# Performance work log

Measured on AMD Instinct MI355X. Metric: run time of the kernel, lower is better.

Reference implementation:

```python
import jax, jax.numpy as jnp
import numpy as np

IS_DECODER = True
NEG = -100000.0


def setup_inputs() -> dict:
    key = jax.random.key(0)
    ks = jax.random.split(key, 8)
    B, S, E, H = 8, 2048, 1024, 64
    return {
        "hidden_state": jax.random.normal(ks[0], (B, S, E), dtype=jnp.float32),
        "attention_masks": jax.random.randint(ks[1], (B, S), 0, 2, dtype=jnp.int32),
        "Wq": jax.random.normal(ks[2], (E, H), dtype=jnp.float32) / np.sqrt(E),
        "bq": jax.random.normal(ks[3], (H,), dtype=jnp.float32) * 0.02,
        "Wk": jax.random.normal(ks[4], (E, H), dtype=jnp.float32) / np.sqrt(E),
        "bk": jax.random.normal(ks[5], (H,), dtype=jnp.float32) * 0.02,
        "Wv": jax.random.normal(ks[6], (E, H), dtype=jnp.float32) / np.sqrt(E),
        "bv": jax.random.normal(ks[7], (H,), dtype=jnp.float32) * 0.02,
    }


def reference(hidden_state, attention_masks, Wq, bq, Wk, bk, Wv, bv):
    # projections: q,k,v [B,S,H]
    q = hidden_state @ Wq + bq
    k = hidden_state @ Wk + bk
    v = hidden_state @ Wv + bv
    dim = q.shape[-1]
    # scores [B,S,S]
    score = jnp.einsum("bqh,bkh->bqk", q, k) / jnp.sqrt(jnp.float32(dim))
    m = attention_masks.astype(score.dtype)  # [B,S]
    pad = 1.0 - m
    amm = m[:, :, None] * m[:, None, :]      # [B,S,S]
    pmm = pad[:, :, None] * pad[:, None, :]
    if IS_DECODER:
        S = m.shape[-1]
        amm = amm * jnp.tril(jnp.ones((S, S), dtype=score.dtype))
    coupling = 1.0 - amm - pmm
    score = score + coupling * NEG
    weights = jax.nn.softmax(score, axis=-1)
    return jnp.einsum("bqk,bkh->bqh", weights, v)
```

## Files before the change

### kernel.cpp

```cpp
#include <hip/hip_runtime.h>

typedef float f32x4 __attribute__((ext_vector_type(4)));
typedef float f32x16 __attribute__((ext_vector_type(16)));
typedef unsigned int u32x4 __attribute__((ext_vector_type(4)));
typedef __bf16 bf16x8 __attribute__((ext_vector_type(8)));
typedef unsigned short ushort_t;

#define NEG2 (-144269.5f)
#define SCLQ (0.18033688f)

constexpr int Ss = 2048, Ee = 1024, Hh = 64;

static __device__ __forceinline__ ushort_t f2bfu(float f) {
  return __builtin_bit_cast(ushort_t, (__bf16)f);
}
static __device__ __forceinline__ f32x4 mfma16(bf16x8 a, bf16x8 b, f32x4 c) {
  return __builtin_amdgcn_mfma_f32_16x16x32_bf16(a, b, c, 0, 0, 0);
}
static __device__ __forceinline__ f32x16 mfma32(bf16x8 a, bf16x8 b, f32x16 c) {
  return __builtin_amdgcn_mfma_f32_32x32x16_bf16(a, b, c, 0, 0, 0);
}
static __device__ __forceinline__ unsigned cvtpk(float a, float b) {
  unsigned r;
  asm("v_cvt_pk_bf16_f32 %0, %1, %2" : "=v"(r) : "v"(a), "v"(b));
  return r;
}
static __device__ __forceinline__ void swap32(unsigned& a, unsigned& b) {
  asm("v_permlane32_swap_b32 %0, %1" : "+v"(a), "+v"(b));
}
static __device__ __forceinline__ void gload_lds16(const void* g, void* l) {
  __builtin_amdgcn_global_load_lds(
      (const __attribute__((address_space(1))) unsigned int*)g,
      (__attribute__((address_space(3))) unsigned int*)l, 16, 0, 0);
}


__global__ __launch_bounds__(256) void k_wtrans(const float* __restrict__ Wq,
                                                const float* __restrict__ Wk,
                                                const float* __restrict__ Wv,
                                                ushort_t* __restrict__ Wsw) {
  __shared__ float tile[64][65];
  const float* W = (blockIdx.y == 0) ? Wq : (blockIdx.y == 1 ? Wk : Wv);
  int kt = blockIdx.x, t = threadIdx.x;
  int r = t >> 2, cq = t & 3;
  const float* src = W + (kt * 64 + r) * Hh + cq * 16;
#pragma unroll
  for (int j = 0; j < 16; j += 4) {
    float4 v = *reinterpret_cast<const float4*>(src + j);
    tile[r][cq * 16 + j + 0] = v.x;
    tile[r][cq * 16 + j + 1] = v.y;
    tile[r][cq * 16 + j + 2] = v.z;
    tile[r][cq * 16 + j + 3] = v.w;
  }
  __syncthreads();
  int n = t >> 2, kq = t & 3;
  int rr = blockIdx.y * 64 + n;
  ushort_t ob[16];
#pragma unroll
  for (int j = 0; j < 16; ++j) ob[j] = f2bfu(tile[kq * 16 + j][n]);
#pragma unroll
  for (int j = 0; j < 2; ++j) {
    int c16 = 2 * kq + j;
    size_t off = ((size_t)(kt * 192 + rr)) * 64 + (size_t)(((c16 ^ (rr & 7))) * 8);
    *reinterpret_cast<uint4*>(Wsw + off) = reinterpret_cast<uint4*>(ob)[j];
  }
}

__global__ __launch_bounds__(256, 2) void k_proj(const float* __restrict__ hs,
                                                 const float* __restrict__ bq,
                                                 const float* __restrict__ bk,
                                                 const float* __restrict__ bv,
                                                 const ushort_t* __restrict__ Wsw,
                                                 const int* __restrict__ am,
                                                 ushort_t* __restrict__ qf_,
                                                 ushort_t* __restrict__ kf_,
                                                 ushort_t* __restrict__ vf_,
                                                 float* __restrict__ pen) {
  __shared__ __align__(16) ushort_t bufA[2][32][72];
  __shared__ __align__(16) ushort_t bufW[2][192 * 64];

  int t = threadIdx.x, w = t >> 6, l = t & 63, g = l >> 4, c = l & 15;
  int wm = w >> 1, wn = w & 1;
  int row0 = blockIdx.x * 32;

  int ar = t >> 3, ach = t & 7;
  const float* agp = hs + (size_t)(row0 + ar) * Ee + ach * 8;

  f32x4 acc[6];
#pragma unroll
  for (int nt = 0; nt < 6; ++nt) acc[nt] = f32x4{0.f, 0.f, 0.f, 0.f};
  float4 aR0, aR1;

  auto LOADA = [&](int kk) {
    aR0 = *reinterpret_cast<const float4*>(agp + kk);
    aR1 = *reinterpret_cast<const float4*>(agp + kk + 4);
  };
  auto WRITEA = [&](int buf) {
    bf16x8 av;
    av[0] = (__bf16)aR0.x; av[1] = (__bf16)aR0.y; av[2] = (__bf16)aR0.z; av[3] = (__bf16)aR0.w;
    av[4] = (__bf16)aR1.x; av[5] = (__bf16)aR1.y; av[6] = (__bf16)aR1.z; av[7] = (__bf16)aR1.w;
    *reinterpret_cast<bf16x8*>(&bufA[buf][ar][ach * 8]) = av;
  };
  auto GLW = [&](int buf, int s) {
    const ushort_t* base = Wsw + (size_t)s * 12288;
#pragma unroll
    for (int j = 0; j < 6; ++j) {
      int seg = j * 4 + w;
      const ushort_t* gp = base + seg * 512 + l * 8;
      gload_lds16(gp, &bufW[buf][seg * 512]);
    }
  };
  auto COMPUTE = [&](int buf) {
    const ushort_t* Ab = &bufA[buf][wm * 16 + c][0];
    bf16x8 af0 = *reinterpret_cast<const bf16x8*>(Ab + g * 8);
    bf16x8 af1 = *reinterpret_cast<const bf16x8*>(Ab + 32 + g * 8);
#pragma unroll
    for (int nt = 0; nt < 6; ++nt) {
      int r = wn * 96 + nt * 16 + c;
      int slot = g ^ (r & 7);
      const ushort_t* Wb = &bufW[buf][r * 64];
      bf16x8 b0 = *reinterpret_cast<const bf16x8*>(Wb + slot * 8);
      bf16x8 b1 = *reinterpret_cast<const bf16x8*>(Wb + (slot ^ 4) * 8);
      acc[nt] = mfma16(af0, b0, acc[nt]);
      acc[nt] = mfma16(af1, b1, acc[nt]);
    }
  };

  LOADA(0);
  WRITEA(0);
  GLW(0, 0);
  LOADA(64);
  __builtin_amdgcn_sched_barrier(0);

  int cur = 0;
  for (int s = 0; s < 16; ++s) {
    __syncthreads();
    if (s < 15) {
      WRITEA(cur ^ 1);
      GLW(cur ^ 1, s + 1);
    }
    if (s < 14) {
      LOADA((s + 2) * 64);
      __builtin_amdgcn_sched_barrier(0);
    }
    COMPUTE(cur);
    cur ^= 1;
  }

#pragma unroll
  for (int nt = 0; nt < 6; ++nt) {
    int T = wn * 6 + nt;
    int m = T >> 2;
    int h = (T & 3) * 16 + c;
    const float* bias = (m == 0) ? bq : ((m == 1) ? bk : bv);
    float bb = bias[h];
    int cc = h >> 4, hh = (h >> 3) & 1, jj = h & 7;
    int dt = h >> 5, dl = h & 31;
#pragma unroll
    for (int i = 0; i < 4; ++i) {
      int row = row0 + wm * 16 + g * 4 + i;
      float val = acc[nt][i] + bb;
      int bi = row >> 11, rl = row & 2047;
      if (m == 0) {
        size_t a = ((((size_t)(bi * 64 + (rl >> 5)) * 4 + cc) * 2 + hh) * 32 + (rl & 31)) * 8 + jj;
        qf_[a] = f2bfu(val * SCLQ);
      } else if (m == 1) {
        size_t a = ((((size_t)(bi * 64 + (rl >> 5)) * 4 + cc) * 2 + hh) * 32 + (rl & 31)) * 8 + jj;
        kf_[a] = f2bfu(val);
      } else {
        int s16 = rl >> 4, vh = (rl >> 3) & 1, vj = rl & 7;
        size_t a = ((((size_t)(bi * 128 + s16) * 2 + dt) * 2 + vh) * 32 + dl) * 8 + vj;
        vf_[a] = f2bfu(val);
      }
    }
  }

  if (t < 32) {
    int grow = row0 + t;
    int bi = grow >> 11, s2 = grow & 2047;
    int mv = am[grow];
    pen[((size_t)bi * 2 + 0) * Ss + s2] = mv ? 0.f : NEG2;
    pen[((size_t)bi * 2 + 1) * Ss + s2] = mv ? NEG2 : 0.f;
  }
}

__global__ __launch_bounds__(256, 2) void k_attn(const ushort_t* __restrict__ qs,
                                                 const ushort_t* __restrict__ km,
                                                 const ushort_t* __restrict__ vm,
                                                 const int* __restrict__ am,
                                                 const float* __restrict__ pen,
                                                 float* __restrict__ opart,
                                                 float* __restrict__ lpart) {
  __shared__ float obuf[4][64][68];
  __shared__ float lls[4][64];

  int t = threadIdx.x, w = t >> 6, l = t & 63, lo = l & 31, hi = l >> 5;
  int bid = blockIdx.x;
  int b = bid & 7, qt2 = (bid >> 3) & 31, kh = bid >> 8;
  int q0A = qt2 * 64, q0B = q0A + 32;

  const size_t laneoff = (size_t)hi * 256 + lo * 8;

  const ushort_t* qbaseA = qs + (size_t)(b * 64 + qt2 * 2) * 2048 + laneoff;
  const ushort_t* qbaseB = qbaseA + 2048;
  bf16x8 qfA[4], qfB[4];
#pragma unroll
  for (int c = 0; c < 4; ++c) {
    qfA[c] = *reinterpret_cast<const bf16x8*>(qbaseA + (size_t)c * 512);
    qfB[c] = *reinterpret_cast<const bf16x8*>(qbaseB + (size_t)c * 512);
  }

  int mqA = am[b * Ss + q0A + lo], mqB = am[b * Ss + q0B + lo];
  float negqA = mqA ? NEG2 : 0.f, negqB = mqB ? NEG2 : 0.f;
  const float* pselA = pen + ((size_t)b * 2 + (mqA ? 0 : 1)) * Ss;
  const float* pselB = pen + ((size_t)b * 2 + (mqB ? 0 : 1)) * Ss;

  float llA = 0.f, llB = 0.f;
  f32x16 o0A = {0.f, 0.f, 0.f, 0.f, 0.f, 0.f, 0.f, 0.f, 0.f, 0.f, 0.f, 0.f, 0.f, 0.f, 0.f, 0.f};
  f32x16 o1A = o0A, o0B = o0A, o1B = o0A;
  const f32x16 z16 = o0A;

  const int kvbeg = kh * 1024 + w * 256;
  const ushort_t* kb = km + (size_t)b * 131072 + laneoff;
  const ushort_t* vb = vm + (size_t)b * 131072 + laneoff;

  for (int it = 0; it < 8; ++it) {
    const int kv0 = kvbeg + it * 32;
    const int kt32 = kv0 >> 5, s16 = kv0 >> 4;

    const ushort_t* kfp = kb + (size_t)kt32 * 2048;
    bf16x8 kf0 = *reinterpret_cast<const bf16x8*>(kfp);
    bf16x8 kf1 = *reinterpret_cast<const bf16x8*>(kfp + 512);
    bf16x8 kf2 = *reinterpret_cast<const bf16x8*>(kfp + 1024);
    bf16x8 kf3 = *reinterpret_cast<const bf16x8*>(kfp + 1536);
    const ushort_t* vfp = vb + (size_t)s16 * 1024;
    bf16x8 vf00 = *reinterpret_cast<const bf16x8*>(vfp);
    bf16x8 vf01 = *reinterpret_cast<const bf16x8*>(vfp + 512);
    bf16x8 vf10 = *reinterpret_cast<const bf16x8*>(vfp + 1024);
    bf16x8 vf11 = *reinterpret_cast<const bf16x8*>(vfp + 1536);

    f32x4 pvA[4];
#pragma unroll
    for (int j = 0; j < 4; ++j)
      pvA[j] = *reinterpret_cast<const f32x4*>(pselA + kv0 + j * 8 + hi * 4);

    f32x16 scA = mfma32(kf0, qfA[0], z16);
    scA = mfma32(kf1, qfA[1], scA);
    scA = mfma32(kf2, qfA[2], scA);
    scA = mfma32(kf3, qfA[3], scA);
    f32x16 scB = mfma32(kf0, qfB[0], z16);
    scB = mfma32(kf1, qfB[1], scB);
    scB = mfma32(kf2, qfB[2], scB);
    scB = mfma32(kf3, qfB[3], scB);

    if (kv0 == q0A) {
#pragma unroll
      for (int r = 0; r < 16; ++r) {
        int kr = (r & 3) + 8 * (r >> 2) + 4 * hi;
        scA[r] += pvA[r >> 2][r & 3] + ((kr > lo) ? negqA : 0.f);
      }
    } else {
      float addt = (kv0 > q0A) ? negqA : 0.f;
#pragma unroll
      for (int r = 0; r < 16; ++r) scA[r] += pvA[r >> 2][r & 3] + addt;
    }
    float pA[16], tsA = 0.f;
#pragma unroll
    for (int r = 0; r < 16; ++r) {
      pA[r] = __builtin_amdgcn_exp2f(scA[r]);
      tsA += pA[r];
    }
    llA += tsA;
    unsigned xa0 = cvtpk(pA[0], pA[1]), ya0 = cvtpk(pA[2], pA[3]);
    unsigned za0 = cvtpk(pA[4], pA[5]), wa0 = cvtpk(pA[6], pA[7]);
    swap32(xa0, za0);
    swap32(ya0, wa0);
    unsigned xa1 = cvtpk(pA[8], pA[9]), ya1 = cvtpk(pA[10], pA[11]);
    unsigned za1 = cvtpk(pA[12], pA[13]), wa1 = cvtpk(pA[14], pA[15]);
    swap32(xa1, za1);
    swap32(ya1, wa1);
    bf16x8 paA0 = __builtin_bit_cast(bf16x8, u32x4{xa0, ya0, za0, wa0});
    bf16x8 paA1 = __builtin_bit_cast(bf16x8, u32x4{xa1, ya1, za1, wa1});
    o0A = mfma32(paA0, vf00, o0A);
    o0A = mfma32(paA1, vf10, o0A);
    o1A = mfma32(paA0, vf01, o1A);
    o1A = mfma32(paA1, vf11, o1A);

    f32x4 pvB[4];
#pragma unroll
    for (int j = 0; j < 4; ++j)
      pvB[j] = *reinterpret_cast<const f32x4*>(pselB + kv0 + j * 8 + hi * 4);

    if (kv0 == q0B) {
#pragma unroll
      for (int r = 0; r < 16; ++r) {
        int kr = (r & 3) + 8 * (r >> 2) + 4 * hi;
        scB[r] += pvB[r >> 2][r & 3] + ((kr > lo) ? negqB : 0.f);
      }
    } else {
      float addt = (kv0 > q0B) ? negqB : 0.f;
#pragma unroll
      for (int r = 0; r < 16; ++r) scB[r] += pvB[r >> 2][r & 3] + addt;
    }
    float pB[16], tsB = 0.f;
#pragma unroll
    for (int r = 0; r < 16; ++r) {
      pB[r] = __builtin_amdgcn_exp2f(scB[r]);
      tsB += pB[r];
    }
    llB += tsB;
    unsigned xb0 = cvtpk(pB[0], pB[1]), yb0 = cvtpk(pB[2], pB[3]);
    unsigned zb0 = cvtpk(pB[4], pB[5]), wb0 = cvtpk(pB[6], pB[7]);
    swap32(xb0, zb0);
    swap32(yb0, wb0);
    unsigned xb1 = cvtpk(pB[8], pB[9]), yb1 = cvtpk(pB[10], pB[11]);
    unsigned zb1 = cvtpk(pB[12], pB[13]), wb1 = cvtpk(pB[14], pB[15]);
    swap32(xb1, zb1);
    swap32(yb1, wb1);
    bf16x8 paB0 = __builtin_bit_cast(bf16x8, u32x4{xb0, yb0, zb0, wb0});
    bf16x8 paB1 = __builtin_bit_cast(bf16x8, u32x4{xb1, yb1, zb1, wb1});
    o0B = mfma32(paB0, vf00, o0B);
    o0B = mfma32(paB1, vf10, o0B);
    o1B = mfma32(paB0, vf01, o1B);
    o1B = mfma32(paB1, vf11, o1B);
  }

  llA += __shfl_xor(llA, 32);
  llB += __shfl_xor(llB, 32);

#pragma unroll
  for (int r = 0; r < 16; ++r) {
    int qrow = (r & 3) + 8 * (r >> 2) + 4 * hi;
    obuf[w][qrow][lo] = o0A[r];
    obuf[w][qrow][32 + lo] = o1A[r];
    obuf[w][32 + qrow][lo] = o0B[r];
    obuf[w][32 + qrow][32 + lo] = o1B[r];
  }
  if (hi == 0) {
    lls[w][lo] = llA;
    lls[w][32 + lo] = llB;
  }
  __syncthreads();

  int qr = t >> 3, dg = t & 7;
#pragma unroll
  for (int pass = 0; pass < 2; ++pass) {
    int row = pass * 32 + qr;
    float lg = lls[0][row] + lls[1][row] + lls[2][row] + lls[3][row];
    float a8[8] = {0.f, 0.f, 0.f, 0.f, 0.f, 0.f, 0.f, 0.f};
#pragma unroll
    for (int ww = 0; ww < 4; ++ww) {
      float4 c0 = *reinterpret_cast<const float4*>(&obuf[ww][row][dg * 8]);
      float4 c1 = *reinterpret_cast<const float4*>(&obuf[ww][row][dg * 8 + 4]);
      a8[0] += c0.x; a8[1] += c0.y; a8[2] += c0.z; a8[3] += c0.w;
      a8[4] += c1.x; a8[5] += c1.y; a8[6] += c1.z; a8[7] += c1.w;
    }
    float* op = opart + (((size_t)kh * 8 + b) * Ss + q0A + row) * 64 + dg * 8;
    float4 r0v = {a8[0], a8[1], a8[2], a8[3]};
    float4 r1v = {a8[4], a8[5], a8[6], a8[7]};
    *reinterpret_cast<float4*>(op) = r0v;
    *reinterpret_cast<float4*>(op + 4) = r1v;
    if (dg == 0) lpart[((size_t)kh * 8 + b) * Ss + q0A + row] = lg;
  }
}

__global__ __launch_bounds__(256) void k_fin(const float* __restrict__ op,
                                             const float* __restrict__ lp,
                                             float* __restrict__ out) {
  int gi = blockIdx.x * 256 + threadIdx.x;
  int row = gi >> 4;
  float lsum = lp[row] + lp[row + 16384];
  f32x4 a = reinterpret_cast<const f32x4*>(op)[gi];
  f32x4 b = reinterpret_cast<const f32x4*>(op)[gi + 262144];
  float inv = 1.f / lsum;
  f32x4 r = (a + b) * inv;
  reinterpret_cast<f32x4*>(out)[gi] = r;
}

extern "C" void kernel_launch(void* const* d_in, const int* in_sizes, int n_in,
                              void* d_out, int out_size, void* d_ws, size_t ws_size,
                              hipStream_t stream) {
  const float* hs = (const float*)d_in[0];
  const int* am = (const int*)d_in[1];
  const float* Wq = (const float*)d_in[2];
  const float* bq = (const float*)d_in[3];
  const float* Wk = (const float*)d_in[4];
  const float* bk = (const float*)d_in[5];
  const float* Wv = (const float*)d_in[6];
  const float* bv = (const float*)d_in[7];
  float* out = (float*)d_out;

  char* ws = (char*)d_ws;
  ushort_t* qsp = (ushort_t*)(ws + 0);
  ushort_t* kp = (ushort_t*)(ws + (2u << 20));
  ushort_t* vtp = (ushort_t*)(ws + (4u << 20));
  ushort_t* wtp = (ushort_t*)(ws + (6u << 20));
  float* penp = (float*)(ws + (6u << 20) + (512u << 10));
  float* opart = (float*)(ws + (8u << 20));
  float* lpart = (float*)(ws + (16u << 20));

  k_wtrans<<<dim3(16, 3), 256, 0, stream>>>(Wq, Wk, Wv, wtp);
  k_proj<<<dim3(512), 256, 0, stream>>>(hs, bq, bk, bv, wtp, am, qsp, kp, vtp, penp);
  k_attn<<<dim3(512), 256, 0, stream>>>(qsp, kp, vtp, am, penp, opart, lpart);
  k_fin<<<dim3(1024), 256, 0, stream>>>(opart, lpart, out);
}
```

Before: 47.36 us.

## Fuse split-KV finalize into attention kernel using 8-wave blocks

Instead of splitting the KV range across two blocks and combining the partial outputs in a separate finalize kernel, each block now runs 8 waves covering the full 2048-long KV range. The partial outputs are reduced in shared memory in two stages, and the normalized result is written directly to the output. This removes one kernel launch and the global round-trip of the partial output and row-sum buffers. In exchange the grid is halved to 256 blocks of 512 threads, which may lower occupancy and adds an extra barrier plus a shared-memory accumulate step.

Measured after the change: 44.70 us (median of 2 runs). 5.6% less time.

```diff
diff --git a/kernel.cpp b/kernel.cpp
--- a/kernel.cpp
+++ b/kernel.cpp
@@ -184,19 +184,18 @@
   }
 }
 
-__global__ __launch_bounds__(256, 2) void k_attn(const ushort_t* __restrict__ qs,
+__global__ __launch_bounds__(512, 2) void k_attn(const ushort_t* __restrict__ qs,
                                                  const ushort_t* __restrict__ km,
                                                  const ushort_t* __restrict__ vm,
                                                  const int* __restrict__ am,
                                                  const float* __restrict__ pen,
-                                                 float* __restrict__ opart,
-                                                 float* __restrict__ lpart) {
+                                                 float* __restrict__ out) {
   __shared__ float obuf[4][64][68];
-  __shared__ float lls[4][64];
+  __shared__ float lls[8][64];
 
   int t = threadIdx.x, w = t >> 6, l = t & 63, lo = l & 31, hi = l >> 5;
   int bid = blockIdx.x;
-  int b = bid & 7, qt2 = (bid >> 3) & 31, kh = bid >> 8;
+  int b = bid & 7, qt2 = bid >> 3;
   int q0A = qt2 * 64, q0B = q0A + 32;
 
   const size_t laneoff = (size_t)hi * 256 + lo * 8;
@@ -220,7 +219,7 @@
   f32x16 o1A = o0A, o0B = o0A, o1B = o0A;
   const f32x16 z16 = o0A;
 
-  const int kvbeg = kh * 1024 + w * 256;
+  const int kvbeg = w * 256;
   const ushort_t* kb = km + (size_t)b * 131072 + laneoff;
   const ushort_t* vb = vm + (size_t)b * 131072 + laneoff;
 
@@ -327,54 +326,52 @@
 
   llA += __shfl_xor(llA, 32);
   llB += __shfl_xor(llB, 32);
-
-#pragma unroll
-  for (int r = 0; r < 16; ++r) {
-    int qrow = (r & 3) + 8 * (r >> 2) + 4 * hi;
-    obuf[w][qrow][lo] = o0A[r];
-    obuf[w][qrow][32 + lo] = o1A[r];
-    obuf[w][32 + qrow][lo] = o0B[r];
-    obuf[w][32 + qrow][32 + lo] = o1B[r];
-  }
   if (hi == 0) {
     lls[w][lo] = llA;
     lls[w][32 + lo] = llB;
   }
+
+  if (w >= 4) {
+#pragma unroll
+    for (int r = 0; r < 16; ++r) {
+      int qrow = (r & 3) + 8 * (r >> 2) + 4 * hi;
+      obuf[w - 4][qrow][lo] = o0A[r];
+      obuf[w - 4][qrow][32 + lo] = o1A[r];
+      obuf[w - 4][32 + qrow][lo] = o0B[r];
+      obuf[w - 4][32 + qrow][32 + lo] = o1B[r];
+    }
+  }
   __syncthreads();
+  if (w < 4) {
+#pragma unroll
+    for (int r = 0; r < 16; ++r) {
+      int qrow = (r & 3) + 8 * (r >> 2) + 4 * hi;
+      obuf[w][qrow][lo] += o0A[r];
+      obuf[w][qrow][32 + lo] += o1A[r];
+      obuf[w][32 + qrow][lo] += o0B[r];
+      obuf[w][32 + qrow][32 + lo] += o1B[r];
+    }
+  }
+  __syncthreads();
 
   int qr = t >> 3, dg = t & 7;
-#pragma unroll
-  for (int pass = 0; pass < 2; ++pass) {
-    int row = pass * 32 + qr;
-    float lg = lls[0][row] + lls[1][row] + lls[2][row] + lls[3][row];
-    float a8[8] = {0.f, 0.f, 0.f, 0.f, 0.f, 0.f, 0.f, 0.f};
-#pragma unroll
-    for (int ww = 0; ww < 4; ++ww) {
-      float4 c0 = *reinterpret_cast<const float4*>(&obuf[ww][row][dg * 8]);
-      float4 c1 = *reinterpret_cast<const float4*>(&obuf[ww][row][dg * 8 + 4]);
-      a8[0] += c0.x; a8[1] += c0.y; a8[2] += c0.z; a8[3] += c0.w;
-      a8[4] += c1.x; a8[5] += c1.y; a8[6] += c1.z; a8[7] += c1.w;
-    }
-    float* op = opart + (((size_t)kh * 8 + b) * Ss + q0A + row) * 64 + dg * 8;
-    float4 r0v = {a8[0], a8[1], a8[2], a8[3]};
-    float4 r1v = {a8[4], a8[5], a8[6], a8[7]};
-    *reinterpret_cast<float4*>(op) = r0v;
-    *reinterpret_cast<float4*>(op + 4) = r1v;
-    if (dg == 0) lpart[((size_t)kh * 8 + b) * Ss + q0A + row] = lg;
-  }
-}
-
-__global__ __launch_bounds__(256) void k_fin(const float* __restrict__ op,
-                                             const float* __restrict__ lp,
-                                             float* __restrict__ out) {
-  int gi = blockIdx.x * 256 + threadIdx.x;
-  int row = gi >> 4;
-  float lsum = lp[row] + lp[row + 16384];
-  f32x4 a = reinterpret_cast<const f32x4*>(op)[gi];
-  f32x4 b = reinterpret_cast<const f32x4*>(op)[gi + 262144];
-  float inv = 1.f / lsum;
-  f32x4 r = (a + b) * inv;
-  reinterpret_cast<f32x4*>(out)[gi] = r;
+  float lg = 0.f;
+#pragma unroll
+  for (int ww = 0; ww < 8; ++ww) lg += lls[ww][qr];
+  float a8[8] = {0.f, 0.f, 0.f, 0.f, 0.f, 0.f, 0.f, 0.f};
+#pragma unroll
+  for (int ww = 0; ww < 4; ++ww) {
+    float4 c0 = *reinterpret_cast<const float4*>(&obuf[ww][qr][dg * 8]);
+    float4 c1 = *reinterpret_cast<const float4*>(&obuf[ww][qr][dg * 8 + 4]);
+    a8[0] += c0.x; a8[1] += c0.y; a8[2] += c0.z; a8[3] += c0.w;
+    a8[4] += c1.x; a8[5] += c1.y; a8[6] += c1.z; a8[7] += c1.w;
+  }
+  float inv = 1.f / lg;
+  float4 r0v = {a8[0] * inv, a8[1] * inv, a8[2] * inv, a8[3] * inv};
+  float4 r1v = {a8[4] * inv, a8[5] * inv, a8[6] * inv, a8[7] * inv};
+  float* op = out + ((size_t)(b * Ss + q0A + qr)) * Hh + dg * 8;
+  *reinterpret_cast<float4*>(op) = r0v;
+  *reinterpret_cast<float4*>(op + 4) = r1v;
 }
 
 extern "C" void kernel_launch(void* const* d_in, const int* in_sizes, int n_in,
@@ -396,11 +393,8 @@
   ushort_t* vtp = (ushort_t*)(ws + (4u << 20));
   ushort_t* wtp = (ushort_t*)(ws + (6u << 20));
   float* penp = (float*)(ws + (6u << 20) + (512u << 10));
-  float* opart = (float*)(ws + (8u << 20));
-  float* lpart = (float*)(ws + (16u << 20));
 
   k_wtrans<<<dim3(16, 3), 256, 0, stream>>>(Wq, Wk, Wv, wtp);
   k_proj<<<dim3(512), 256, 0, stream>>>(hs, bq, bk, bv, wtp, am, qsp, kp, vtp, penp);
-  k_attn<<<dim3(512), 256, 0, stream>>>(qsp, kp, vtp, am, penp, opart, lpart);
-  k_fin<<<dim3(1024), 256, 0, stream>>>(opart, lpart, out);
-}
+  k_attn<<<dim3(256), 512, 0, stream>>>(qsp, kp, vtp, am, penp, out);
+}
```
